# Kernel tuning notes

Measured on AMD Instinct MI355X. Metric: run time of the kernel, lower is better.

The kernel has to match this reference:

```python
import jax, jax.numpy as jnp
from jax import lax
import numpy as np

H = 48; W = 48; C_IN = 256; A_PER = 3
M = A_PER * H * W            # 6912 anchors
IMG = 768.0                  # square image, clip bound for x and y
OBJ_THR = 0.3; IOU_THR = 0.7; TOP_K = 2000
NEG = -1e9                   # finite sentinel for masked scores


def _make_anchors():
    stride = IMG / H
    base = 2.0 * stride
    ratios = np.array([0.5, 1.0, 2.0])
    ws = base * np.sqrt(ratios)          # [3]
    hs = base / np.sqrt(ratios)
    cx = (np.arange(W) + 0.5) * stride
    cy = (np.arange(H) + 0.5) * stride
    cxg, cyg = np.meshgrid(cx, cy)       # [H, W]
    anc = np.stack([
        cxg[None] - ws[:, None, None] / 2,
        cyg[None] - hs[:, None, None] / 2,
        cxg[None] + ws[:, None, None] / 2,
        cyg[None] + hs[:, None, None] / 2,
    ], axis=-1)                           # [3, H, W, 4] matches (anchor, h, w) flatten order
    return jnp.asarray(anc.reshape(-1, 4), jnp.float32)


def setup_inputs() -> dict:
    key = jax.random.key(0)
    ks = jax.random.split(key, 4)
    x = jax.random.normal(ks[0], (1, C_IN, H, W), jnp.float32)
    conv_w = jax.random.normal(ks[1], (256, 256, 3, 3), jnp.float32) * 0.02
    conv_b = jnp.zeros((256,), jnp.float32)
    det_w = jax.random.normal(ks[2], (3, 256, 1, 1), jnp.float32) * 0.02
    det_b = jnp.zeros((3,), jnp.float32)
    reg_w = jax.random.normal(ks[3], (12, 256, 1, 1), jnp.float32) * 0.02
    reg_b = jnp.zeros((12,), jnp.float32)
    anchors = _make_anchors()
    return {"x": x, "conv_w": conv_w, "conv_b": conv_b, "det_w": det_w,
            "det_b": det_b, "reg_w": reg_w, "reg_b": reg_b, "anchors": anchors}


def reference(x, conv_w, conv_b, det_w, det_b, reg_w, reg_b, anchors):
    # ---- FPN 3x3 conv + RPN head (1x1 convs) ----
    inter = lax.conv_general_dilated(
        x, conv_w, (1, 1), 'SAME',
        dimension_numbers=('NCHW', 'OIHW', 'NCHW')) + conv_b[None, :, None, None]
    obj = jax.nn.sigmoid(jnp.einsum('nchw,oc->nohw', inter, det_w[:, :, 0, 0])
                         + det_b[None, :, None, None])          # [1,3,H,W]
    reg = (jnp.einsum('nchw,oc->nohw', inter, reg_w[:, :, 0, 0])
           + reg_b[None, :, None, None])                        # [1,12,H,W]

    scores = obj.reshape(-1)                                    # [M], (anchor,h,w) order
    deltas = reg.reshape(1, 4, A_PER, H, W).transpose(0, 2, 3, 4, 1).reshape(-1, 4)

    # ---- box decode (preserves the source's cx/cy quirk: cx = y1 + w/2, cy = x1 + h/2) ----
    x1, y1, x2, y2 = anchors[:, 0], anchors[:, 1], anchors[:, 2], anchors[:, 3]
    aw = x2 - x1; ah = y2 - y1
    acx = y1 + aw / 2; acy = x1 + ah / 2
    dx, dy, dw, dh = deltas[:, 0], deltas[:, 1], deltas[:, 2], deltas[:, 3]
    px = acx + dx * aw; py = acy + dy * ah
    pw = aw * jnp.exp(dw); ph = ah * jnp.exp(dh)
    boxes = jnp.stack([px - pw / 2, py - ph / 2, px + pw / 2, py + ph / 2], axis=-1)

    # ---- clip to image ----
    boxes = jnp.clip(boxes, 0.0, IMG)

    # ---- validity: degenerate filter (source's naming quirk) + objectness threshold ----
    hts = boxes[:, 2] - boxes[:, 0]
    wds = boxes[:, 3] - boxes[:, 1]
    valid = (hts > 0) & (wds > 0) & (scores > OBJ_THR)

    # ---- greedy NMS (jit-friendly: sort, pairwise IoU, sequential suppression) ----
    s = jnp.where(valid, scores, NEG)
    order = jnp.argsort(-s)
    b = boxes[order]; v = valid[order]; ss = s[order]
    area = (b[:, 2] - b[:, 0]) * (b[:, 3] - b[:, 1])             # [M]
    iw = jnp.clip(jnp.minimum(b[:, None, 2], b[None, :, 2])
                  - jnp.maximum(b[:, None, 0], b[None, :, 0]), 0.0)
    ih = jnp.clip(jnp.minimum(b[:, None, 3], b[None, :, 3])
                  - jnp.maximum(b[:, None, 1], b[None, :, 1]), 0.0)
    inter_a = iw * ih                                             # [M,M]
    iou = inter_a / jnp.maximum(area[:, None] + area[None, :] - inter_a, 1e-9)

    idx = jnp.arange(M)

    def body(suppressed, i):
        keep_i = v[i] & (~suppressed[i])
        sup = keep_i & (iou[i] > IOU_THR) & (idx > i)
        return suppressed | sup, keep_i

    _, keeps = lax.scan(body, jnp.zeros(M, bool), idx)            # keep mask (sorted order)

    # ---- top-k proposal selection (fixed K, padded with sentinels) ----
    out_s = jnp.where(keeps, ss, NEG)
    topv, topi = lax.top_k(out_s, TOP_K)
    vtop = keeps[topi]
    out_scores = jnp.where(vtop, topv, -1.0)                      # [TOP_K]
    out_boxes = jnp.where(vtop[:, None], b[topi], 0.0)            # [TOP_K, 4]
    return out_scores, out_boxes
```

## Files before the change

### kernel.cpp

```cpp
#include <hip/hip_runtime.h>
#include <cstdint>

#define NPX 2304
#define MM 6912
#define NW 108
#define TOPK 2000
#define NEGV -1000000000.0f
#define OBJ_THRF 0.3f
#define IOU_THRF 0.7f
#define IMGF 768.0f
#define KSPLIT 4

typedef unsigned long long u64;
typedef unsigned int u32;

__device__ __forceinline__ u64 shfl64(u64 v, int src) {
  int lo = __shfl((int)(v & 0xffffffffull), src, 64);
  int hi = __shfl((int)(v >> 32), src, 64);
  return ((u64)(u32)hi << 32) | (u32)lo;
}

__global__ __launch_bounds__(256) void k_wt(const float* __restrict__ cw,
                                            float* __restrict__ wt) {
  __shared__ float t[64][65];
  const int it0 = blockIdx.x * 64;
  const int oc0 = blockIdx.y * 64;
  const int tx = threadIdx.x & 63;
  const int ty = threadIdx.x >> 6;
#pragma unroll
  for (int k = 0; k < 16; ++k) {
    int oc = ty + k * 4;
    t[oc][tx] = cw[(oc0 + oc) * 2304 + it0 + tx];
  }
  __syncthreads();
#pragma unroll
  for (int k = 0; k < 16; ++k) {
    int it = ty + k * 4;
    wt[(it0 + it) * 256 + oc0 + tx] = t[tx][it];
  }
}

__global__ __launch_bounds__(256) void k_conv(const float* __restrict__ x,
                                              const float* __restrict__ wt,
                                              float* __restrict__ part) {
  __shared__ float xs[16 * 8 * 52];
  const int tid = threadIdx.x;
  const int px = blockIdx.x * 256 + tid;
  const int oc0 = blockIdx.y * 16;
  const int ks = blockIdx.z;
  const int row = px / 48, col = px % 48;
  const int r0 = (blockIdx.x * 256) / 48;
  const int rbase = row - r0;

  float acc[16];
#pragma unroll
  for (int k = 0; k < 16; ++k) acc[k] = 0.f;

  for (int icc = 0; icc < 64 / 16; ++icc) {
    const int ic0 = ks * 64 + icc * 16;
    for (int e = tid; e < 16 * 8 * 50; e += 256) {
      int ic = e / 400, rem = e % 400;
      int r = rem / 50, c = rem % 50 - 1;
      int gr = r0 - 1 + r;
      float v = 0.f;
      if (c >= 0 && c < 48 && gr >= 0 && gr < 48)
        v = x[(ic0 + ic) * NPX + gr * 48 + c];
      xs[(ic * 8 + r) * 52 + (c + 1)] = v;
    }
    __syncthreads();
    for (int ic = 0; ic < 16; ++ic) {
      float xv[9];
#pragma unroll
      for (int dr = 0; dr < 3; ++dr)
#pragma unroll
        for (int dc = 0; dc < 3; ++dc)
          xv[dr * 3 + dc] = xs[(ic * 8 + rbase + dr) * 52 + col + dc];
      const float* wrow = wt + (size_t)(ic0 + ic) * 9 * 256 + oc0;
#pragma unroll
      for (int t = 0; t < 9; ++t) {
        const float* wp = wrow + t * 256;
#pragma unroll
        for (int k = 0; k < 16; ++k) acc[k] += xv[t] * wp[k];
      }
    }
    __syncthreads();
  }
#pragma unroll
  for (int k = 0; k < 16; ++k)
    part[((size_t)ks * 256 + oc0 + k) * NPX + px] = acc[k];
}

__global__ __launch_bounds__(256) void k_decode(const float* __restrict__ part,
                                                const float* __restrict__ cb,
                                                const float* __restrict__ dw,
                                                const float* __restrict__ db,
                                                const float* __restrict__ rw,
                                                const float* __restrict__ rb,
                                                const float* __restrict__ anch,
                                                float* __restrict__ s,
                                                float4* __restrict__ boxes) {
  __shared__ float wl[256 * 16];
  const int tid = threadIdx.x;
  const int p = blockIdx.x * 256 + tid;
  for (int e = tid; e < 3840; e += 256) {
    int o = e % 15, c = e / 15;
    wl[c * 16 + o] = (o < 3) ? dw[o * 256 + c] : rw[(o - 3) * 256 + c];
  }
  __syncthreads();
  float acc[15];
#pragma unroll
  for (int o = 0; o < 15; o++) acc[o] = 0.f;
  for (int c = 0; c < 256; ++c) {
    float v = cb[c];
#pragma unroll
    for (int kks = 0; kks < KSPLIT; ++kks)
      v += part[((size_t)kks * 256 + c) * NPX + p];
#pragma unroll
    for (int o = 0; o < 15; o++) acc[o] += v * wl[c * 16 + o];
  }
  const float4* an4 = (const float4*)anch;
#pragma unroll
  for (int a = 0; a < 3; ++a) {
    int m = a * NPX + p;
    float logit = acc[a] + db[a];
    float score = 1.f / (1.f + expf(-logit));
    float dxv = acc[3 + 0 + a] + rb[0 + a];
    float dyv = acc[3 + 3 + a] + rb[3 + a];
    float dwv = acc[3 + 6 + a] + rb[6 + a];
    float dhv = acc[3 + 9 + a] + rb[9 + a];
    float4 an = an4[m];
    float aw = an.z - an.x;
    float ah = an.w - an.y;
    float acx = an.y + aw * 0.5f;
    float acy = an.x + ah * 0.5f;
    float pxc = acx + dxv * aw;
    float pyc = acy + dyv * ah;
    float pw = aw * expf(dwv);
    float ph = ah * expf(dhv);
    float b0 = pxc - pw * 0.5f, b1 = pyc - ph * 0.5f;
    float b2 = pxc + pw * 0.5f, b3 = pyc + ph * 0.5f;
    b0 = fminf(fmaxf(b0, 0.f), IMGF);
    b1 = fminf(fmaxf(b1, 0.f), IMGF);
    b2 = fminf(fmaxf(b2, 0.f), IMGF);
    b3 = fminf(fmaxf(b3, 0.f), IMGF);
    float hts = b2 - b0, wds = b3 - b1;
    bool valid = (hts > 0.f) && (wds > 0.f) && (score > OBJ_THRF);
    s[m] = valid ? score : NEGV;
    boxes[m] = make_float4(b0, b1, b2, b3);
  }
}

__global__ __launch_bounds__(256) void k_sortA(const float* __restrict__ s,
                                               u64* __restrict__ keys) {
  __shared__ u64 lds[1024];
  const int tid = threadIdx.x;
  const int b = blockIdx.x;
  for (int v = tid; v < 1024; v += 256) {
    int i = b * 1024 + v;
    u64 p;
    if (i < MM) {
      u32 u = __float_as_uint(s[i]);
      u = u ^ (u32)(((int)u >> 31) | 0x80000000);
      p = ((u64)(~u) << 32) | (u32)i;
    } else {
      p = ~0ull;
    }
    lds[v] = p;
  }
  for (u32 kk = 2; kk <= 1024; kk <<= 1) {
    for (u32 j = kk >> 1; j > 0; j >>= 1) {
      __syncthreads();
#pragma unroll 2
      for (int t = tid; t < 512; t += 256) {
        int i = ((t & ~(j - 1)) << 1) | (t & (j - 1));
        int l = i | j;
        bool up = ((i & kk) == 0);
        u64 a = lds[i], c = lds[l];
        u64 mn = a < c ? a : c;
        u64 mx = a < c ? c : a;
        lds[i] = up ? mn : mx;
        lds[l] = up ? mx : mn;
      }
    }
  }
  __syncthreads();
  for (int v = tid; v < 1024; v += 256) keys[b * 1024 + v] = lds[v];
}

__global__ __launch_bounds__(256) void k_merge(const u64* __restrict__ in,
                                               u64* __restrict__ outk, int L, int fin,
                                               const float* __restrict__ s,
                                               const float4* __restrict__ boxes,
                                               float* __restrict__ ssc,
                                               float4* __restrict__ sboxes) {
  const int i = blockIdx.x * 256 + threadIdx.x;
  const int pair = i / (2 * L);
  const int r = i - pair * 2 * L;
  const u64* A = in + (size_t)pair * 2 * L;
  const u64* B = A + L;
  int lo = (r > L) ? (r - L) : 0;
  int hi = (r < L) ? r : L;
  while (lo < hi) {
    int mid = (lo + hi) >> 1;
    if (A[mid] < B[r - 1 - mid]) lo = mid + 1; else hi = mid;
  }
  int a = lo, bi = r - lo;
  u64 av = (a < L) ? A[a] : ~0ull;
  u64 bv = (bi < L) ? B[bi] : ~0ull;
  u64 o = (av < bv) ? av : bv;
  outk[i] = o;
  if (fin && i < MM) {
    int idx = (int)(u32)o;
    ssc[i] = s[idx];
    sboxes[i] = boxes[idx];
  }
}

__global__ __launch_bounds__(256) void k_zero(u64* __restrict__ nz) {
  int i = blockIdx.x * 256 + threadIdx.x;
  if (i < MM * 2) nz[i] = 0;
}

__global__ __launch_bounds__(256) void k_mask(const float4* __restrict__ sboxes,
                                              u64* __restrict__ mask_t,
                                              u64* __restrict__ nz) {
  __shared__ float4 rb_[64];
  const int rt = blockIdx.x;
  const int w = blockIdx.y * 4 + (threadIdx.x >> 6);
  const int lane = threadIdx.x & 63;
  if (threadIdx.x < 64) rb_[threadIdx.x] = sboxes[rt * 64 + threadIdx.x];
  __syncthreads();
  if (w < rt) return;
  float4 c = sboxes[w * 64 + lane];
  float areaC = (c.z - c.x) * (c.w - c.y);
  u64 myw = 0;
  for (int r = 0; r < 64; ++r) {
    float4 b = rb_[r];
    float iw = fmaxf(fminf(b.z, c.z) - fmaxf(b.x, c.x), 0.f);
    float ih = fmaxf(fminf(b.w, c.w) - fmaxf(b.y, c.y), 0.f);
    float inter = iw * ih;
    float areaB = (b.z - b.x) * (b.w - b.y);
    float un = fmaxf(areaB + areaC - inter, 1e-9f);
    bool bit = (inter / un) > IOU_THRF;
    u64 bal = __ballot(bit);
    if (lane == r) myw = bal;
  }
  mask_t[(size_t)w * MM + rt * 64 + lane] = myw;
  if (myw) atomicOr(&nz[(rt * 64 + lane) * 2 + (w >> 6)], 1ull << (w & 63));
}

__global__ __launch_bounds__(256) void k_scan(const u64* __restrict__ mask_t,
                                              const u64* __restrict__ nz,
                                              const float* __restrict__ ssc,
                                              const float4* __restrict__ sboxes,
                                              float* __restrict__ out) {
  __shared__ u64 remv[NW];
  __shared__ u64 keepw[NW];
  __shared__ int blist[64];
  __shared__ int nkS;
  __shared__ int kcntS;
  __shared__ int pref[NW];
  const int tid = threadIdx.x;
  if (tid < NW) { remv[tid] = 0; keepw[tid] = 0; }
  if (tid == 0) kcntS = 0;
  __syncthreads();

  for (int c = 0; c < NW; ++c) {
    if (tid < 64) {
      const int lane = tid;
      u64 dg = mask_t[(size_t)c * MM + c * 64 + lane];
      float sv = ssc[c * 64 + lane];
      u64 vb = __ballot(sv > OBJ_THRF);
      u64 w0 = remv[c];
      u64 cand = vb & ~w0;
      u64 above = (lane < 63) ? ~((2ull << lane) - 1ull) : 0ull;
      bool inC = ((cand >> lane) & 1ull) != 0;
      u64 conf = __ballot(inC && ((dg & above & cand) != 0ull));
      u64 kb;
      if (conf == 0ull) {
        kb = cand;
      } else {
        u64 w = w0;
        kb = 0;
        u64 rem = cand;
        while (rem) {
          int b = __ffsll(rem) - 1;
          kb |= (1ull << b);
          w |= shfl64(dg, b);
          rem = vb & ~w;
        }
      }
      int below = __popcll(kb & ((1ull << lane) - 1ull));
      if ((kb >> lane) & 1ull) blist[below] = lane;
      if (lane == 0) {
        keepw[c] = kb;
        nkS = __popcll(kb);
        kcntS += __popcll(kb);
      }
    }
    __syncthreads();
    int nk = nkS;
    if (tid < nk) {
      int row = c * 64 + blist[tid];
      u64 nz0 = nz[row * 2], nz1 = nz[row * 2 + 1];
      if (c < 64) {
        nz0 &= (c < 63) ? ~((2ull << c) - 1ull) : 0ull;
      } else {
        nz0 = 0;
        int cc = c - 64;
        nz1 &= ~((2ull << cc) - 1ull);
      }
      while (nz0) {
        int wv = __ffsll(nz0) - 1; nz0 &= nz0 - 1;
        atomicOr(&remv[wv], mask_t[(size_t)wv * MM + row]);
      }
      while (nz1) {
        int wv = __ffsll(nz1) - 1; nz1 &= nz1 - 1;
        atomicOr(&remv[wv + 64], mask_t[(size_t)(wv + 64) * MM + row]);
      }
    }
    __syncthreads();
    if (kcntS >= TOPK) break;
  }

  if (tid == 0) {
    int run = 0;
    for (int cc = 0; cc < NW; ++cc) { pref[cc] = run; run += __popcll(keepw[cc]); }
  }
  __syncthreads();
  for (int e = tid; e < TOPK * 5; e += 256) out[e] = (e < TOPK) ? -1.0f : 0.0f;
  __syncthreads();
  float4* ob = (float4*)(out + TOPK);
  for (int i = tid; i < MM; i += 256) {
    int cc = i >> 6, b = i & 63;
    u64 kb = keepw[cc];
    if ((kb >> b) & 1ull) {
      int rank = pref[cc] + __popcll(kb & ((1ull << b) - 1ull));
      if (rank < TOPK) {
        out[rank] = ssc[i];
        ob[rank] = sboxes[i];
      }
    }
  }
}

extern "C" void kernel_launch(void* const* d_in, const int* in_sizes, int n_in,
                              void* d_out, int out_size, void* d_ws, size_t ws_size,
                              hipStream_t stream) {
  const float* x  = (const float*)d_in[0];
  const float* cw = (const float*)d_in[1];
  const float* cb = (const float*)d_in[2];
  const float* dw = (const float*)d_in[3];
  const float* db = (const float*)d_in[4];
  const float* rw = (const float*)d_in[5];
  const float* rb = (const float*)d_in[6];
  const float* an = (const float*)d_in[7];
  char* ws = (char*)d_ws;
  float*  part   = (float*)(ws);
  u64*    keysA  = (u64*)(ws);
  u64*    keysB  = (u64*)(ws + 65536);
  u64*    mask   = (u64*)(ws);
  u64*    nz     = (u64*)(ws + 5971968);
  float*  wt     = (float*)(ws + 9437184);
  float*  s      = (float*)(ws + 11796480);
  float4* boxes  = (float4*)(ws + 11824128);
  float*  ssc    = (float*)(ws + 11934720);
  float4* sboxes = (float4*)(ws + 11962368);
  float* out = (float*)d_out;

  hipLaunchKernelGGL(k_wt, dim3(36, 4), dim3(256), 0, stream, cw, wt);
  hipLaunchKernelGGL(k_conv, dim3(9, 16, KSPLIT), dim3(256), 0, stream, x, wt, part);
  hipLaunchKernelGGL(k_decode, dim3(9), dim3(256), 0, stream, part, cb, dw, db, rw, rb, an, s, boxes);
  hipLaunchKernelGGL(k_zero, dim3(54), dim3(256), 0, stream, nz);
  hipLaunchKernelGGL(k_sortA, dim3(8), dim3(256), 0, stream, s, keysA);
  hipLaunchKernelGGL(k_merge, dim3(32), dim3(256), 0, stream, keysA, keysB, 1024, 0, s, boxes, ssc, sboxes);
  hipLaunchKernelGGL(k_merge, dim3(32), dim3(256), 0, stream, keysB, keysA, 2048, 0, s, boxes, ssc, sboxes);
  hipLaunchKernelGGL(k_merge, dim3(32), dim3(256), 0, stream, keysA, keysB, 4096, 1, s, boxes, ssc, sboxes);
  hipLaunchKernelGGL(k_mask, dim3(108, 27), dim3(256), 0, stream, sboxes, mask, nz);
  hipLaunchKernelGGL(k_scan, dim3(1), dim3(256), 0, stream, mask, nz, ssc, sboxes, out);
}
```

Baseline: 332.6 us.

## Double conv split-K and parallelize decode across channel quarters

Raises the split-K factor of the 3x3 conv from 4 to 8, so 1152 blocks run instead of 576 and each block handles 32 input channels. The decode kernel now spreads the 256-channel reduction over four thread groups per 64 pixels and combines them through shared memory, launching 36 blocks instead of 9. Workspace offsets move to fit the larger partial buffer. The cost is twice the partial-sum traffic written by the conv and read by decode, plus an LDS reduction step.

```diff
diff --git a/kernel.cpp b/kernel.cpp
--- a/kernel.cpp
+++ b/kernel.cpp
@@ -9,7 +9,7 @@
 #define OBJ_THRF 0.3f
 #define IOU_THRF 0.7f
 #define IMGF 768.0f
-#define KSPLIT 4
+#define KSPLIT 8
 
 typedef unsigned long long u64;
 typedef unsigned int u32;
@@ -56,8 +56,8 @@
 #pragma unroll
   for (int k = 0; k < 16; ++k) acc[k] = 0.f;
 
-  for (int icc = 0; icc < 64 / 16; ++icc) {
-    const int ic0 = ks * 64 + icc * 16;
+  for (int icc = 0; icc < 2; ++icc) {
+    const int ic0 = ks * 32 + icc * 16;
     for (int e = tid; e < 16 * 8 * 50; e += 256) {
       int ic = e / 400, rem = e % 400;
       int r = rem / 50, c = rem % 50 - 1;
@@ -100,8 +100,11 @@
                                                 float* __restrict__ s,
                                                 float4* __restrict__ boxes) {
   __shared__ float wl[256 * 16];
+  __shared__ float red[4 * 64 * 17];
   const int tid = threadIdx.x;
-  const int p = blockIdx.x * 256 + tid;
+  const int pxl = tid & 63;
+  const int cq = tid >> 6;
+  const int px = blockIdx.x * 64 + pxl;
   for (int e = tid; e < 3840; e += 256) {
     int o = e % 15, c = e / 15;
     wl[c * 16 + o] = (o < 3) ? dw[o * 256 + c] : rw[(o - 3) * 256 + c];
@@ -110,43 +113,55 @@
   float acc[15];
 #pragma unroll
   for (int o = 0; o < 15; o++) acc[o] = 0.f;
-  for (int c = 0; c < 256; ++c) {
+  for (int ci = 0; ci < 64; ++ci) {
+    int c = cq * 64 + ci;
     float v = cb[c];
 #pragma unroll
     for (int kks = 0; kks < KSPLIT; ++kks)
-      v += part[((size_t)kks * 256 + c) * NPX + p];
+      v += part[((size_t)kks * 256 + c) * NPX + px];
 #pragma unroll
     for (int o = 0; o < 15; o++) acc[o] += v * wl[c * 16 + o];
   }
-  const float4* an4 = (const float4*)anch;
-#pragma unroll
-  for (int a = 0; a < 3; ++a) {
-    int m = a * NPX + p;
-    float logit = acc[a] + db[a];
-    float score = 1.f / (1.f + expf(-logit));
-    float dxv = acc[3 + 0 + a] + rb[0 + a];
-    float dyv = acc[3 + 3 + a] + rb[3 + a];
-    float dwv = acc[3 + 6 + a] + rb[6 + a];
-    float dhv = acc[3 + 9 + a] + rb[9 + a];
-    float4 an = an4[m];
-    float aw = an.z - an.x;
-    float ah = an.w - an.y;
-    float acx = an.y + aw * 0.5f;
-    float acy = an.x + ah * 0.5f;
-    float pxc = acx + dxv * aw;
-    float pyc = acy + dyv * ah;
-    float pw = aw * expf(dwv);
-    float ph = ah * expf(dhv);
-    float b0 = pxc - pw * 0.5f, b1 = pyc - ph * 0.5f;
-    float b2 = pxc + pw * 0.5f, b3 = pyc + ph * 0.5f;
-    b0 = fminf(fmaxf(b0, 0.f), IMGF);
-    b1 = fminf(fmaxf(b1, 0.f), IMGF);
-    b2 = fminf(fmaxf(b2, 0.f), IMGF);
-    b3 = fminf(fmaxf(b3, 0.f), IMGF);
-    float hts = b2 - b0, wds = b3 - b1;
-    bool valid = (hts > 0.f) && (wds > 0.f) && (score > OBJ_THRF);
-    s[m] = valid ? score : NEGV;
-    boxes[m] = make_float4(b0, b1, b2, b3);
+#pragma unroll
+  for (int o = 0; o < 15; o++) red[(cq * 64 + pxl) * 17 + o] = acc[o];
+  __syncthreads();
+  if (tid < 64) {
+    const int p = blockIdx.x * 64 + tid;
+    float a[15];
+#pragma unroll
+    for (int o = 0; o < 15; o++)
+      a[o] = red[tid * 17 + o] + red[(64 + tid) * 17 + o] +
+             red[(128 + tid) * 17 + o] + red[(192 + tid) * 17 + o];
+    const float4* an4 = (const float4*)anch;
+#pragma unroll
+    for (int aa = 0; aa < 3; ++aa) {
+      int m = aa * NPX + p;
+      float logit = a[aa] + db[aa];
+      float score = 1.f / (1.f + expf(-logit));
+      float dxv = a[3 + 0 + aa] + rb[0 + aa];
+      float dyv = a[3 + 3 + aa] + rb[3 + aa];
+      float dwv = a[3 + 6 + aa] + rb[6 + aa];
+      float dhv = a[3 + 9 + aa] + rb[9 + aa];
+      float4 an = an4[m];
+      float aw = an.z - an.x;
+      float ah = an.w - an.y;
+      float acx = an.y + aw * 0.5f;
+      float acy = an.x + ah * 0.5f;
+      float pxc = acx + dxv * aw;
+      float pyc = acy + dyv * ah;
+      float pw = aw * expf(dwv);
+      float ph = ah * expf(dhv);
+      float b0 = pxc - pw * 0.5f, b1 = pyc - ph * 0.5f;
+      float b2 = pxc + pw * 0.5f, b3 = pyc + ph * 0.5f;
+      b0 = fminf(fmaxf(b0, 0.f), IMGF);
+      b1 = fminf(fmaxf(b1, 0.f), IMGF);
+      b2 = fminf(fmaxf(b2, 0.f), IMGF);
+      b3 = fminf(fmaxf(b3, 0.f), IMGF);
+      float hts = b2 - b0, wds = b3 - b1;
+      bool valid = (hts > 0.f) && (wds > 0.f) && (score > OBJ_THRF);
+      s[m] = valid ? score : NEGV;
+      boxes[m] = make_float4(b0, b1, b2, b3);
+    }
   }
 }
 
@@ -361,16 +376,16 @@
   u64*    keysB  = (u64*)(ws + 65536);
   u64*    mask   = (u64*)(ws);
   u64*    nz     = (u64*)(ws + 5971968);
-  float*  wt     = (float*)(ws + 9437184);
-  float*  s      = (float*)(ws + 11796480);
-  float4* boxes  = (float4*)(ws + 11824128);
-  float*  ssc    = (float*)(ws + 11934720);
-  float4* sboxes = (float4*)(ws + 11962368);
+  float*  wt     = (float*)(ws + 18874368);
+  float*  s      = (float*)(ws + 21233664);
+  float4* boxes  = (float4*)(ws + 21261312);
+  float*  ssc    = (float*)(ws + 21371904);
+  float4* sboxes = (float4*)(ws + 21399552);
   float* out = (float*)d_out;
 
   hipLaunchKernelGGL(k_wt, dim3(36, 4), dim3(256), 0, stream, cw, wt);
   hipLaunchKernelGGL(k_conv, dim3(9, 16, KSPLIT), dim3(256), 0, stream, x, wt, part);
-  hipLaunchKernelGGL(k_decode, dim3(9), dim3(256), 0, stream, part, cb, dw, db, rw, rb, an, s, boxes);
+  hipLaunchKernelGGL(k_decode, dim3(36), dim3(256), 0, stream, part, cb, dw, db, rw, rb, an, s, boxes);
   hipLaunchKernelGGL(k_zero, dim3(54), dim3(256), 0, stream, nz);
   hipLaunchKernelGGL(k_sortA, dim3(8), dim3(256), 0, stream, s, keysA);
   hipLaunchKernelGGL(k_merge, dim3(32), dim3(256), 0, stream, keysA, keysB, 1024, 0, s, boxes, ssc, sboxes);
```

Result: faster. 267.5 us (-19.6%).
